# Kernel tuning notes

Measured on AMD Instinct MI355X. Metric: run time of the kernel, lower is better.

Reference implementation:

```python
import jax, jax.numpy as jnp
import numpy as np


def _conv1x1(w, x):
    # w: [out, in], x: [B, in, H, W] -> [B, out, H, W]
    return jnp.einsum('oc,bchw->bohw', w, x)


def _maxpool2(x):
    # 2x2 max pool, stride 2. x: [B, C, H, W] -> [B, C, H//2, W//2]
    B, C, H, W = x.shape
    return x.reshape(B, C, H // 2, 2, W // 2, 2).max(axis=(3, 5))


def setup_inputs() -> dict:
    key = jax.random.key(0)
    ks = jax.random.split(key, 5)
    B, C, H, W = 8, 256, 64, 64
    div = 8
    x = jax.random.normal(ks[0], (B, C, H, W), dtype=jnp.float32)
    wq = jax.random.normal(ks[1], (C // div, C), dtype=jnp.float32) * (C ** -0.5)
    wk = jax.random.normal(ks[2], (C // div, C), dtype=jnp.float32) * (C ** -0.5)
    wv = jax.random.normal(ks[3], (C // 2, C), dtype=jnp.float32) * (C ** -0.5)
    wo = jax.random.normal(ks[4], (C, C // 2), dtype=jnp.float32) * ((C // 2) ** -0.5)
    gamma = jnp.float32(0.5)  # nonzero so attention branch contributes
    return {"x": x, "wq": wq, "wk": wk, "wv": wv, "wo": wo, "gamma": gamma}


def reference(x, wq, wk, wv, wo, gamma):
    B, C, H, W = x.shape
    HW = H * W
    # query: [B, HW, Cq]
    q = _conv1x1(wq, x).reshape(B, -1, HW).transpose(0, 2, 1)
    # key: maxpool -> [B, Cq, HW//4]
    k = _maxpool2(_conv1x1(wk, x)).reshape(B, -1, HW // 4)
    # value: maxpool -> [B, C//2, HW//4]
    v = _maxpool2(_conv1x1(wv, x)).reshape(B, -1, HW // 4)
    scores = jnp.einsum('bnc,bcm->bnm', q, k)          # [B, HW, HW//4]
    attn = jax.nn.softmax(scores, axis=2)
    ctx = jnp.einsum('bcm,bnm->bcn', v, attn)          # [B, C//2, HW]
    ctx = ctx.reshape(B, C // 2, H, W)
    out = gamma * _conv1x1(wo, ctx) + x
    return out
```

## Files before the change

kernel.cpp:

```cpp
#include <hip/hip_runtime.h>
#include <hip/hip_bf16.h>

#define BB  8
#define CC  256
#define HW  4096
#define CQ  32
#define CV  128
#define MP  1024

#define XT_OFF  0
#define Y_OFF   4194304
#define KT_OFF  (Y_OFF + 3145728)
#define VP_OFF  (KT_OFF + 131072)
#define CT_OFF  (VP_OFF + 524288)

typedef __attribute__((ext_vector_type(8))) short bf16x8;
typedef __attribute__((ext_vector_type(4))) short short4v;
typedef __attribute__((ext_vector_type(4))) float f32x4;

__device__ __forceinline__ short f2b(float f) {
    unsigned u = __float_as_uint(f);
    u += 0x7fffu + ((u >> 16) & 1u);
    return (short)(u >> 16);
}
__device__ __forceinline__ float b2f(short s) {
    return __uint_as_float(((unsigned)(unsigned short)s) << 16);
}

__global__ __launch_bounds__(256) void k_xt(
    const float* __restrict__ x, short* __restrict__ xt)
{
    __shared__ float t[64][65];
    const int bid = blockIdx.x;
    const int nt = bid & 63;
    const int ct = (bid >> 6) & 3;
    const int b  = bid >> 8;
    const int c0 = ct * 64, n0 = nt * 64;
    const int tid = threadIdx.x;

    const int col = tid & 63, wrow = (tid >> 6) * 16;
    #pragma unroll
    for (int i = 0; i < 16; ++i) {
        int r = wrow + i;
        t[r][col] = x[((long)(b * CC + c0 + r)) * HW + n0 + col];
    }
    __syncthreads();

    const int n = tid >> 2, cb = (tid & 3) * 16;
    short buf[16];
    #pragma unroll
    for (int j = 0; j < 16; ++j) buf[j] = f2b(t[cb + j][n]);
    short* dst = &xt[((long)(b * HW + n0 + n)) * CC + c0 + cb];
    *(int4*)dst = *(int4*)&buf[0];
    *(int4*)(dst + 8) = *(int4*)&buf[8];
}

__global__ __launch_bounds__(256) void k_qkv(
    const float* __restrict__ wq, const float* __restrict__ wk,
    const float* __restrict__ wv, const short* __restrict__ xt,
    short* __restrict__ y)
{
    __shared__ short w_lds[96 * 264];
    __shared__ short x_lds[256 * 40];
    const int bid = blockIdx.x;
    const int oc = bid & 1;
    const int nt = (bid >> 1) & 15;
    const int b  = bid >> 5;
    const int o0 = oc * 96, n0 = nt * 256;
    const int tid = threadIdx.x;
    const int lane = tid & 63;
    const int wvid = tid >> 6;
    const int l15 = lane & 15, g = lane >> 4;

    for (int it = 0; it < 24; ++it) {
        int idx = tid + it * 256;
        int ol = idx >> 6, cq = (idx & 63) * 4;
        int o = o0 + ol;
        const float* src = (o < 32) ? &wq[o * 256 + cq]
                         : (o < 64) ? &wk[(o - 32) * 256 + cq]
                                    : &wv[(o - 64) * 256 + cq];
        float4 w = *(const float4*)src;
        short4v p = { f2b(w.x), f2b(w.y), f2b(w.z), f2b(w.w) };
        *(short4v*)&w_lds[ol * 264 + cq] = p;
    }

    f32x4 acc[4][6];
    #pragma unroll
    for (int nf = 0; nf < 4; ++nf)
        #pragma unroll
        for (int of = 0; of < 6; ++of) acc[nf][of] = (f32x4){0.f, 0.f, 0.f, 0.f};

    for (int ks = 0; ks < 8; ++ks) {
        __syncthreads();
        {
            const short* src = &xt[((long)(b * HW + n0 + tid)) * CC + ks * 32];
            int4 v0 = *(const int4*)src;
            int4 v1 = *(const int4*)(src + 8);
            int4 v2 = *(const int4*)(src + 16);
            int4 v3 = *(const int4*)(src + 24);
            short* dst = &x_lds[tid * 40];
            *(int4*)dst = v0; *(int4*)(dst + 8) = v1;
            *(int4*)(dst + 16) = v2; *(int4*)(dst + 24) = v3;
        }
        __syncthreads();

        bf16x8 a[4], bf[6];
        #pragma unroll
        for (int nf = 0; nf < 4; ++nf)
            a[nf] = *(const bf16x8*)&x_lds[(wvid * 64 + nf * 16 + l15) * 40 + 8 * g];
        #pragma unroll
        for (int of = 0; of < 6; ++of)
            bf[of] = *(const bf16x8*)&w_lds[(of * 16 + l15) * 264 + ks * 32 + 8 * g];
        #pragma unroll
        for (int nf = 0; nf < 4; ++nf)
            #pragma unroll
            for (int of = 0; of < 6; ++of)
                acc[nf][of] = __builtin_amdgcn_mfma_f32_16x16x32_bf16(a[nf], bf[of], acc[nf][of], 0, 0, 0);
    }

    #pragma unroll
    for (int nf = 0; nf < 4; ++nf) {
        #pragma unroll
        for (int of = 0; of < 6; ++of) {
            int o = o0 + of * 16 + l15;
            long nb = (long)(b * HW + n0 + wvid * 64 + nf * 16 + 4 * g);
            #pragma unroll
            for (int r = 0; r < 4; ++r)
                y[(nb + r) * 192 + o] = f2b(acc[nf][of][r]);
        }
    }
}

__global__ __launch_bounds__(256) void k_pool(
    const short* __restrict__ y, short* __restrict__ kT, short* __restrict__ vp)
{
    __shared__ short t[64 * 136];
    const int bid = blockIdx.x;
    const int mt = bid & 15;
    const int b  = bid >> 4;
    const int m0 = mt * 64;
    const int tid = threadIdx.x;

    {
        int ml = tid >> 2, ci = (tid & 3) * 8;
        int pp = m0 + ml;
        int ph = pp >> 5, pw = pp & 31;
        const short* src = &y[((long)(b * HW) + ph * 128 + pw * 2) * 192 + 32 + ci];
        int4 s0 = *(const int4*)src;
        int4 s1 = *(const int4*)(src + 192);
        int4 s2 = *(const int4*)(src + 12288);
        int4 s3 = *(const int4*)(src + 12480);
        const short *a = (const short*)&s0, *bb = (const short*)&s1,
                    *c = (const short*)&s2, *d = (const short*)&s3;
        short o8[8];
        #pragma unroll
        for (int j = 0; j < 8; ++j)
            o8[j] = f2b(fmaxf(fmaxf(b2f(a[j]), b2f(bb[j])), fmaxf(b2f(c[j]), b2f(d[j]))));
        *(int4*)&kT[((long)(b * MP + pp)) * CQ + ci] = *(int4*)o8;
    }
    #pragma unroll
    for (int jj = 0; jj < 4; ++jj) {
        int idx = tid + jj * 256;
        int ml = idx >> 4, ci = (idx & 15) * 8;
        int pp = m0 + ml;
        int ph = pp >> 5, pw = pp & 31;
        const short* src = &y[((long)(b * HW) + ph * 128 + pw * 2) * 192 + 64 + ci];
        int4 s0 = *(const int4*)src;
        int4 s1 = *(const int4*)(src + 192);
        int4 s2 = *(const int4*)(src + 12288);
        int4 s3 = *(const int4*)(src + 12480);
        const short *a = (const short*)&s0, *bb = (const short*)&s1,
                    *c = (const short*)&s2, *d = (const short*)&s3;
        short o8[8];
        #pragma unroll
        for (int j = 0; j < 8; ++j)
            o8[j] = f2b(fmaxf(fmaxf(b2f(a[j]), b2f(bb[j])), fmaxf(b2f(c[j]), b2f(d[j]))));
        *(int4*)&t[ml * 136 + ci] = *(int4*)o8;
    }
    __syncthreads();
    {
        int c = tid & 127, mc = (tid >> 7) * 32;
        short buf[32];
        #pragma unroll
        for (int mm = 0; mm < 32; ++mm) buf[mm] = t[(mc + mm) * 136 + c];
        short* dst = &vp[((long)(b * CV + c)) * MP + m0 + mc];
        *(int4*)dst = *(int4*)&buf[0];
        *(int4*)(dst + 8)  = *(int4*)&buf[8];
        *(int4*)(dst + 16) = *(int4*)&buf[16];
        *(int4*)(dst + 24) = *(int4*)&buf[24];
    }
}

__global__ __launch_bounds__(128) void k_attn(
    const short* __restrict__ y,
    const short* __restrict__ kT,
    const short* __restrict__ vp,
    short* __restrict__ ctx)
{
    __shared__ short p_lds[2][2][16][40];
    const int tid  = threadIdx.x;
    const int lane = tid & 63;
    const int wid  = tid >> 6;
    const int b    = blockIdx.x >> 6;
    const int q0   = (blockIdx.x & 63) * 64 + wid * 32;
    const int l15  = lane & 15;
    const int g    = lane >> 4;

    bf16x8 qf[2];
    const short* yq = y + (long)b * HW * 192;
    #pragma unroll
    for (int si = 0; si < 2; ++si)
        qf[si] = *(const bf16x8*)&yq[(long)(q0 + si * 16 + l15) * 192 + 8 * g];

    float m_run[2] = {-INFINITY, -INFINITY};
    float l_run[2] = {0.f, 0.f};
    f32x4 acc[2][8];
    #pragma unroll
    for (int si = 0; si < 2; ++si)
        #pragma unroll
        for (int ct = 0; ct < 8; ++ct)
            acc[si][ct] = (f32x4){0.f, 0.f, 0.f, 0.f};

    const short* kTb = kT + (long)b * MP * CQ;
    const short* vpb = vp + (long)b * CV * MP;

    for (int mt = 0; mt < 32; ++mt) {
        const int m0 = mt * 32;
        bf16x8 ka0 = *(const bf16x8*)&kTb[(m0 + l15) * CQ + 8 * g];
        bf16x8 ka1 = *(const bf16x8*)&kTb[(m0 + 16 + l15) * CQ + 8 * g];
        bf16x8 va[8];
        #pragma unroll
        for (int ct = 0; ct < 8; ++ct)
            va[ct] = *(const bf16x8*)&vpb[(ct * 16 + l15) * MP + m0 + 8 * g];

        #pragma unroll
        for (int si = 0; si < 2; ++si) {
            f32x4 s0 = (f32x4){0.f, 0.f, 0.f, 0.f};
            f32x4 s1 = (f32x4){0.f, 0.f, 0.f, 0.f};
            s0 = __builtin_amdgcn_mfma_f32_16x16x32_bf16(ka0, qf[si], s0, 0, 0, 0);
            s1 = __builtin_amdgcn_mfma_f32_16x16x32_bf16(ka1, qf[si], s1, 0, 0, 0);
            float tmax8 = fmaxf(fmaxf(fmaxf(s0[0], s0[1]), fmaxf(s0[2], s0[3])),
                                fmaxf(fmaxf(s1[0], s1[1]), fmaxf(s1[2], s1[3])));
            float mr = m_run[si];
            if (!__all(tmax8 <= mr + 8.0f)) {
                float tmax = fmaxf(tmax8, __shfl_xor(tmax8, 16, 64));
                tmax = fmaxf(tmax, __shfl_xor(tmax, 32, 64));
                float nm    = fmaxf(mr, tmax);
                float alpha = __expf(mr - nm);
                l_run[si] *= alpha;
                #pragma unroll
                for (int r = 0; r < 4; ++r) {
                    float ar = __shfl(alpha, 4 * g + r, 64);
                    #pragma unroll
                    for (int ct = 0; ct < 8; ++ct) acc[si][ct][r] *= ar;
                }
                m_run[si] = nm;
                mr = nm;
            }
            float p[8];
            #pragma unroll
            for (int r = 0; r < 4; ++r) { p[r] = __expf(s0[r] - mr); p[4 + r] = __expf(s1[r] - mr); }
            l_run[si] += ((p[0] + p[1]) + (p[2] + p[3])) + ((p[4] + p[5]) + (p[6] + p[7]));
            short4v w0 = { f2b(p[0]), f2b(p[1]), f2b(p[2]), f2b(p[3]) };
            short4v w1 = { f2b(p[4]), f2b(p[5]), f2b(p[6]), f2b(p[7]) };
            *(short4v*)&p_lds[wid][si][l15][4 * g]      = w0;
            *(short4v*)&p_lds[wid][si][l15][16 + 4 * g] = w1;
        }
        #pragma unroll
        for (int si = 0; si < 2; ++si) {
            bf16x8 pf = *(const bf16x8*)&p_lds[wid][si][l15][8 * g];
            #pragma unroll
            for (int ct = 0; ct < 8; ++ct)
                acc[si][ct] = __builtin_amdgcn_mfma_f32_16x16x32_bf16(pf, va[ct], acc[si][ct], 0, 0, 0);
        }
    }

    #pragma unroll
    for (int si = 0; si < 2; ++si) {
        l_run[si] += __shfl_xor(l_run[si], 16, 64);
        l_run[si] += __shfl_xor(l_run[si], 32, 64);
    }

    #pragma unroll
    for (int si = 0; si < 2; ++si) {
        float inv = 1.f / l_run[si];
        #pragma unroll
        for (int r = 0; r < 4; ++r) {
            float invr = __shfl(inv, 4 * g + r, 64);
            long q = q0 + si * 16 + 4 * g + r;
            short* cb = &ctx[((long)b * HW + q) * CV];
            #pragma unroll
            for (int ct = 0; ct < 8; ++ct)
                cb[ct * 16 + l15] = f2b(acc[si][ct][r] * invr);
        }
    }
}

__global__ __launch_bounds__(256) void k_out(
    const short* __restrict__ ctx, const float* __restrict__ wo,
    const float* __restrict__ x, const float* __restrict__ gamma,
    float* __restrict__ out)
{
    __shared__ short c_lds[256 * 136];
    __shared__ short w_lds[128 * 136];
    const int bid = blockIdx.x;
    const int oc = bid & 1;
    const int nt = (bid >> 1) & 15;
    const int b  = bid >> 5;
    const int o0 = oc * 128, n0 = nt * 256;
    const int tid = threadIdx.x;
    const int lane = tid & 63;
    const int l15 = lane & 15, g = lane >> 4;

    {
        const short* src = &ctx[((long)(b * HW + n0 + tid)) * CV];
        short* dst = &c_lds[tid * 136];
        #pragma unroll
        for (int j = 0; j < 16; ++j)
            *(int4*)(dst + 8 * j) = *(const int4*)(src + 8 * j);
    }
    for (int it = 0; it < 16; ++it) {
        int idx = tid + it * 256;
        int ol = idx >> 5, cq = (idx & 31) * 4;
        float4 w = *(const float4*)&wo[(o0 + ol) * CV + cq];
        short4v p = { f2b(w.x), f2b(w.y), f2b(w.z), f2b(w.w) };
        *(short4v*)&w_lds[ol * 136 + cq] = p;
    }
    __syncthreads();

    const int wvid = tid >> 6;
    const int ow = (wvid & 1) * 64, nw = (wvid >> 1) * 128;
    f32x4 acc[4][8];
    #pragma unroll
    for (int of = 0; of < 4; ++of)
        #pragma unroll
        for (int nf = 0; nf < 8; ++nf) acc[of][nf] = (f32x4){0.f, 0.f, 0.f, 0.f};

    #pragma unroll
    for (int ks = 0; ks < 4; ++ks) {
        bf16x8 af[4], bf[8];
        #pragma unroll
        for (int of = 0; of < 4; ++of)
            af[of] = *(const bf16x8*)&w_lds[(ow + of * 16 + l15) * 136 + ks * 32 + 8 * g];
        #pragma unroll
        for (int nf = 0; nf < 8; ++nf)
            bf[nf] = *(const bf16x8*)&c_lds[(nw + nf * 16 + l15) * 136 + ks * 32 + 8 * g];
        #pragma unroll
        for (int of = 0; of < 4; ++of)
            #pragma unroll
            for (int nf = 0; nf < 8; ++nf)
                acc[of][nf] = __builtin_amdgcn_mfma_f32_16x16x32_bf16(af[of], bf[nf], acc[of][nf], 0, 0, 0);
    }

    const float gma = gamma[0];
    #pragma unroll
    for (int of = 0; of < 4; ++of) {
        #pragma unroll
        for (int r = 0; r < 4; ++r) {
            int o = o0 + ow + of * 16 + 4 * g + r;
            #pragma unroll
            for (int nf = 0; nf < 8; ++nf) {
                int n = n0 + nw + nf * 16 + l15;
                long idx = (long)(b * CC + o) * HW + n;
                out[idx] = gma * acc[of][nf][r] + x[idx];
            }
        }
    }
}

extern "C" void kernel_launch(void* const* d_in, const int* in_sizes, int n_in,
                              void* d_out, int out_size, void* d_ws, size_t ws_size,
                              hipStream_t stream) {
    const float* x     = (const float*)d_in[0];
    const float* wq    = (const float*)d_in[1];
    const float* wk    = (const float*)d_in[2];
    const float* wv    = (const float*)d_in[3];
    const float* wo    = (const float*)d_in[4];
    const float* gamma = (const float*)d_in[5];
    float* out = (float*)d_out;
    float* ws  = (float*)d_ws;

    short* xt  = (short*)(ws + XT_OFF);
    short* y   = (short*)(ws + Y_OFF);
    short* kT  = (short*)(ws + KT_OFF);
    short* vp  = (short*)(ws + VP_OFF);
    short* ctx = (short*)(ws + CT_OFF);

    k_xt  <<<dim3(2048), dim3(256), 0, stream>>>(x, xt);
    k_qkv <<<dim3(256),  dim3(256), 0, stream>>>(wq, wk, wv, xt, y);
    k_pool<<<dim3(128),  dim3(256), 0, stream>>>(y, kT, vp);
    k_attn<<<dim3(512),  dim3(128), 0, stream>>>(y, kT, vp, ctx);
    k_out <<<dim3(256),  dim3(256), 0, stream>>>(ctx, wo, x, gamma, out);
}
```

Baseline: 96.54 us.

## Split attention over key dimension in two halves and merge partial results

The attention kernel now processes half of the pooled keys per block and launches twice as many blocks. Each block writes an unnormalized-then-locally-normalized partial context plus its row max and sum. A new combine kernel merges the two partials using log-sum-exp weights. The goal is more parallelism and better latency hiding in the attention stage, at the cost of extra partial-buffer traffic and one more kernel launch.

New measurement: 96.39 us. No clear change (-0.2%).

```diff
diff --git a/kernel.cpp b/kernel.cpp
--- a/kernel.cpp
+++ b/kernel.cpp
@@ -13,6 +13,9 @@
 #define KT_OFF  (Y_OFF + 3145728)
 #define VP_OFF  (KT_OFF + 131072)
 #define CT_OFF  (VP_OFF + 524288)
+#define P0_OFF  CT_OFF
+#define P1_OFF  XT_OFF
+#define ML_OFF  (XT_OFF + 2097152)
 
 typedef __attribute__((ext_vector_type(8))) short bf16x8;
 typedef __attribute__((ext_vector_type(4))) short short4v;
@@ -195,16 +198,20 @@
     const short* __restrict__ y,
     const short* __restrict__ kT,
     const short* __restrict__ vp,
-    short* __restrict__ ctx)
+    short* __restrict__ p0,
+    short* __restrict__ p1,
+    float* __restrict__ ml)
 {
     __shared__ short p_lds[2][2][16][40];
-    const int tid  = threadIdx.x;
-    const int lane = tid & 63;
-    const int wid  = tid >> 6;
-    const int b    = blockIdx.x >> 6;
-    const int q0   = (blockIdx.x & 63) * 64 + wid * 32;
-    const int l15  = lane & 15;
-    const int g    = lane >> 4;
+    const int tid   = threadIdx.x;
+    const int lane  = tid & 63;
+    const int wid   = tid >> 6;
+    const int split = blockIdx.x >> 9;
+    const int rem   = blockIdx.x & 511;
+    const int b     = rem >> 6;
+    const int q0    = (rem & 63) * 64 + wid * 32;
+    const int l15   = lane & 15;
+    const int g     = lane >> 4;
 
     bf16x8 qf[2];
     const short* yq = y + (long)b * HW * 192;
@@ -224,8 +231,8 @@
     const short* kTb = kT + (long)b * MP * CQ;
     const short* vpb = vp + (long)b * CV * MP;
 
-    for (int mt = 0; mt < 32; ++mt) {
-        const int m0 = mt * 32;
+    for (int mt = 0; mt < 16; ++mt) {
+        const int m0 = split * 512 + mt * 32;
         bf16x8 ka0 = *(const bf16x8*)&kTb[(m0 + l15) * CQ + 8 * g];
         bf16x8 ka1 = *(const bf16x8*)&kTb[(m0 + 16 + l15) * CQ + 8 * g];
         bf16x8 va[8];
@@ -281,6 +288,7 @@
         l_run[si] += __shfl_xor(l_run[si], 32, 64);
     }
 
+    short* pp = split ? p1 : p0;
     #pragma unroll
     for (int si = 0; si < 2; ++si) {
         float inv = 1.f / l_run[si];
@@ -288,12 +296,45 @@
         for (int r = 0; r < 4; ++r) {
             float invr = __shfl(inv, 4 * g + r, 64);
             long q = q0 + si * 16 + 4 * g + r;
-            short* cb = &ctx[((long)b * HW + q) * CV];
+            short* cb = &pp[((long)b * HW + q) * CV];
             #pragma unroll
             for (int ct = 0; ct < 8; ++ct)
                 cb[ct * 16 + l15] = f2b(acc[si][ct][r] * invr);
         }
     }
+    if (lane < 16) {
+        #pragma unroll
+        for (int si = 0; si < 2; ++si) {
+            long row = (long)(split * BB + b) * HW + q0 + si * 16 + lane;
+            ml[row * 2]     = m_run[si];
+            ml[row * 2 + 1] = l_run[si];
+        }
+    }
+}
+
+__global__ __launch_bounds__(256) void k_comb(
+    const short* __restrict__ p0, const short* __restrict__ p1,
+    const float* __restrict__ ml, short* __restrict__ ctx)
+{
+    const long idx = (long)blockIdx.x * 256 + threadIdx.x;
+    const long row = idx >> 4;
+    const int  c0  = (int)(idx & 15) * 8;
+    const float m0 = ml[row * 2],                      l0 = ml[row * 2 + 1];
+    const float m1 = ml[((long)BB * HW + row) * 2],    l1 = ml[((long)BB * HW + row) * 2 + 1];
+    const float M  = fmaxf(m0, m1);
+    float w0 = l0 * __expf(m0 - M);
+    float w1 = l1 * __expf(m1 - M);
+    const float inv = 1.f / (w0 + w1);
+    w0 *= inv; w1 *= inv;
+    int4 a4 = *(const int4*)&p0[row * CV + c0];
+    int4 b4 = *(const int4*)&p1[row * CV + c0];
+    const short* as = (const short*)&a4;
+    const short* bs = (const short*)&b4;
+    short o8[8];
+    #pragma unroll
+    for (int j = 0; j < 8; ++j)
+        o8[j] = f2b(w0 * b2f(as[j]) + w1 * b2f(bs[j]));
+    *(int4*)&ctx[row * CV + c0] = *(int4*)o8;
 }
 
 __global__ __launch_bounds__(256) void k_out(
@@ -385,10 +426,14 @@
     short* kT  = (short*)(ws + KT_OFF);
     short* vp  = (short*)(ws + VP_OFF);
     short* ctx = (short*)(ws + CT_OFF);
+    short* p0  = (short*)(ws + P0_OFF);
+    short* p1  = (short*)(ws + P1_OFF);
+    float* mlb = ws + ML_OFF;
 
     k_xt  <<<dim3(2048), dim3(256), 0, stream>>>(x, xt);
     k_qkv <<<dim3(256),  dim3(256), 0, stream>>>(wq, wk, wv, xt, y);
     k_pool<<<dim3(128),  dim3(256), 0, stream>>>(y, kT, vp);
-    k_attn<<<dim3(512),  dim3(128), 0, stream>>>(y, kT, vp, ctx);
+    k_attn<<<dim3(1024), dim3(128), 0, stream>>>(y, kT, vp, p0, p1, mlb);
+    k_comb<<<dim3(2048), dim3(256), 0, stream>>>(p0, p1, mlb, ctx);
     k_out <<<dim3(256),  dim3(256), 0, stream>>>(ctx, wo, x, gamma, out);
 }
```
